# Kernel optimization log

Hardware: AMD Instinct MI355X
Metric: run time of the kernel (lower is better)

Reference implementation:

```python
import jax, jax.numpy as jnp
import numpy as np

NUM_HEADS = 16
LN_EPS = 1e-5


def setup_inputs() -> dict:
    key = jax.random.key(0)
    ks = jax.random.split(key, 12)
    B, S, D = 4, 2048, 1024
    inp = {
        "query": jax.random.normal(ks[0], (B, S, D), jnp.float32),
        "key": jax.random.normal(ks[1], (B, S, D), jnp.float32),
        "value": jax.random.normal(ks[2], (B, S, D), jnp.float32),
        "mask": jax.random.randint(ks[3], (B, S, S), 0, 2).astype(bool),
        "Wq": 0.02 * jax.random.normal(ks[4], (D, D), jnp.float32),
        "bq": jnp.zeros((D,), jnp.float32),
        "Wk": 0.02 * jax.random.normal(ks[5], (D, D), jnp.float32),
        "bk": jnp.zeros((D,), jnp.float32),
        "Wv": 0.02 * jax.random.normal(ks[6], (D, D), jnp.float32),
        "bv": jnp.zeros((D,), jnp.float32),
        "Wo": 0.02 * jax.random.normal(ks[7], (D, D), jnp.float32),
        "bo": jnp.zeros((D,), jnp.float32),
        "gamma": jnp.ones((D,), jnp.float32),
        "beta": jnp.zeros((D,), jnp.float32),
    }
    return inp


def reference(query, key, value, mask, Wq, bq, Wk, bk, Wv, bv, Wo, bo, gamma, beta):
    B, Sq, D = query.shape
    H = NUM_HEADS
    dk = D // H
    inv_sqrt_dk = 1.0 / float(np.sqrt(dk))

    def proj(x, W, bias):
        # (B, S, D) -> (B, H, S, dk)
        y = x @ W.T + bias
        return y.reshape(B, -1, H, dk).transpose(0, 2, 1, 3)

    Q = proj(query, Wq, bq)
    K = proj(key, Wk, bk)
    V = proj(value, Wv, bv)

    scores = jnp.einsum('bhqd,bhkd->bhqk', Q, K) * inv_sqrt_dk
    scores = jnp.where(mask[:, None, :, :], -jnp.inf, scores)
    attn = jax.nn.softmax(scores, axis=-1)  # (B, H, Sq, Sk)

    ctx = jnp.einsum('bhqk,bhkd->bhqd', attn, V)
    ctx = ctx.transpose(0, 2, 1, 3).reshape(B, Sq, D)

    out = ctx @ Wo.T + bo + query  # residual
    mean = out.mean(-1, keepdims=True)
    var = out.var(-1, keepdims=True)
    output = gamma * (out - mean) * jax.lax.rsqrt(var + LN_EPS) + beta

    # original returns attn flattened head-major: (H*B, Sq, Sk)
    attn_hm = attn.transpose(1, 0, 2, 3).reshape(B * H, Sq, -1)
    return output, attn_hm
```

## Files before the change

kernel.cpp:

```cpp
#include <hip/hip_runtime.h>
#include <hip/hip_bf16.h>
#include <math.h>
#include <stdint.h>

typedef __bf16 bf16_t;
typedef __bf16 bf16x8 __attribute__((ext_vector_type(8)));
typedef __bf16 bf16x4v __attribute__((ext_vector_type(4)));
typedef float f32x4 __attribute__((ext_vector_type(4)));

#define BB 4
#define SS 2048
#define DD 1024
#define HH 16
#define SCALE 0.125f
static constexpr size_t NE = (size_t)BB * SS * DD;
static constexpr size_t WN = (size_t)DD * DD;

__device__ inline f32x4 load4f(const bf16_t* p) {
    bf16x4v v = *(const bf16x4v*)p;
    return (f32x4){(float)v[0], (float)v[1], (float)v[2], (float)v[3]};
}
__device__ inline f32x4 load4f(const float* p) { return *(const f32x4*)p; }
__device__ inline void store4(bf16_t* p, f32x4 v) {
    bf16x4v o;
    for (int j = 0; j < 4; ++j) o[j] = (bf16_t)v[j];
    *(bf16x4v*)p = o;
}
__device__ inline void store4(float* p, f32x4 v) { *(f32x4*)p = v; }
__device__ inline void store16(bf16_t* p, const bf16_t* s) {
    *(bf16x8*)p       = *(const bf16x8*)s;
    *(bf16x8*)(p + 8) = *(const bf16x8*)(s + 8);
}
__device__ inline void store16(float* p, const bf16_t* s) {
    for (int j = 0; j < 16; j += 4) {
        f32x4 v = {(float)s[j], (float)s[j + 1], (float)s[j + 2], (float)s[j + 3]};
        *(f32x4*)(p + j) = v;
    }
}
__device__ inline void cvt8(const float* s, bf16_t* d) {
    f32x4 a = *(const f32x4*)s;
    f32x4 b = *(const f32x4*)(s + 4);
    bf16x8 r;
    for (int j = 0; j < 4; ++j) { r[j] = (bf16_t)a[j]; r[4 + j] = (bf16_t)b[j]; }
    *(bf16x8*)d = r;
}
__device__ __forceinline__ void async16(const bf16_t* g, bf16_t* l) {
    __builtin_amdgcn_global_load_lds(
        (const __attribute__((address_space(1))) void*)g,
        (__attribute__((address_space(3))) void*)l, 16, 0, 0);
}
__device__ __forceinline__ float dpp_max16(float x) {
    x = fmaxf(x, __int_as_float(__builtin_amdgcn_update_dpp(0, __float_as_int(x), 0xB1,  0xF, 0xF, true)));
    x = fmaxf(x, __int_as_float(__builtin_amdgcn_update_dpp(0, __float_as_int(x), 0x4E,  0xF, 0xF, true)));
    x = fmaxf(x, __int_as_float(__builtin_amdgcn_update_dpp(0, __float_as_int(x), 0x141, 0xF, 0xF, true)));
    x = fmaxf(x, __int_as_float(__builtin_amdgcn_update_dpp(0, __float_as_int(x), 0x140, 0xF, 0xF, true)));
    return x;
}
__device__ __forceinline__ float dpp_add16(float x) {
    x += __int_as_float(__builtin_amdgcn_update_dpp(0, __float_as_int(x), 0xB1,  0xF, 0xF, true));
    x += __int_as_float(__builtin_amdgcn_update_dpp(0, __float_as_int(x), 0x4E,  0xF, 0xF, true));
    x += __int_as_float(__builtin_amdgcn_update_dpp(0, __float_as_int(x), 0x141, 0xF, 0xF, true));
    x += __int_as_float(__builtin_amdgcn_update_dpp(0, __float_as_int(x), 0x140, 0xF, 0xF, true));
    return x;
}

__global__ void probe_kernel(const uint16_t* __restrict__ q,
                             const uint8_t* __restrict__ m,
                             int* __restrict__ flags)
{
    __shared__ int s_f32, s_byte, s_i32;
    if (threadIdx.x == 0) { s_f32 = 0; s_byte = 0; s_i32 = 0; }
    __syncthreads();
    {
        unsigned bits = ((unsigned)q[threadIdx.x]) << 16;
        float f = __uint_as_float(bits);
        if (!(fabsf(f) < 1e10f)) atomicOr(&s_f32, 1);
    }
    for (int j = threadIdx.x; j < 4096; j += 256) {
        if (m[j]) {
            if (j & 3) atomicOr(&s_byte, 1);
            else if ((j & 7) == 4) atomicOr(&s_i32, 1);
        }
    }
    __syncthreads();
    if (threadIdx.x == 0) {
        flags[0] = s_f32 ? 1 : 0;
        flags[1] = s_byte ? 0 : (s_i32 ? 1 : 2);
    }
}

__global__ __launch_bounds__(256) void cvt_qkv(
    const float* __restrict__ q, const float* __restrict__ k,
    const float* __restrict__ v, bf16_t* __restrict__ dst,
    const int* __restrict__ flags)
{
    if (flags[0] != 1) return;
    size_t i = ((size_t)blockIdx.x * 256 + threadIdx.x) * 8;
    const float* src;
    size_t off;
    if (i < NE)          { src = q; off = i; }
    else if (i < 2 * NE) { src = k; off = i - NE; }
    else                 { src = v; off = i - 2 * NE; }
    cvt8(src + off, dst + i);
}

__global__ __launch_bounds__(256) void cvt_w(
    const float* __restrict__ Wq, const float* __restrict__ Wk,
    const float* __restrict__ Wv, const float* __restrict__ Wo,
    const float* __restrict__ bq, const float* __restrict__ bk,
    const float* __restrict__ bv, const float* __restrict__ bo,
    bf16_t* __restrict__ dst, const int* __restrict__ flags)
{
    if (flags[0] != 1) return;
    size_t i = ((size_t)blockIdx.x * 256 + threadIdx.x) * 8;
    const float* src;
    size_t off;
    const size_t W4 = 4 * WN;
    if (i < W4) {
        int ws = (int)(i >> 20);
        src = ws == 0 ? Wq : ws == 1 ? Wk : ws == 2 ? Wv : Wo;
        off = i & (WN - 1);
    } else {
        size_t j = i - W4;
        int bs = (int)(j >> 10);
        src = bs == 0 ? bq : bs == 1 ? bk : bs == 2 ? bv : bo;
        off = j & 1023;
    }
    cvt8(src + off, dst + i);
}

template<int BIAS_ROW>
__global__ __launch_bounds__(256) void gemm_bt_bias(
    const bf16_t* __restrict__ A, const bf16_t* __restrict__ B,
    const bf16_t* __restrict__ bias, bf16_t* __restrict__ Y,
    int M, int N, int K, const int* __restrict__ flags, int want)
{
    if (flags[0] != want) return;

    __shared__ __align__(16) bf16_t As[128 * 64];
    __shared__ __align__(16) bf16_t Bs[128 * 64];

    const int tid = threadIdx.x;
    const int wave = tid >> 6;
    const int lane = tid & 63;
    const int quad = lane >> 4;
    const int l15  = lane & 15;
    const int wm = wave >> 1, wn = wave & 1;

    const int m0 = blockIdx.y * 128;
    const int n0 = blockIdx.x * 128;

    f32x4 acc[4][4];
    #pragma unroll
    for (int i = 0; i < 4; ++i)
        #pragma unroll
        for (int j = 0; j < 4; ++j)
            acc[i][j] = (f32x4){0.f, 0.f, 0.f, 0.f};

    for (int k0 = 0; k0 < K; k0 += 64) {
        __syncthreads();
        #pragma unroll
        for (int s = 0; s < 4; ++s) {
            int c = s * 256 + wave * 64 + lane;
            int row = c >> 3, col = (c & 7) * 8;
            bf16_t* la = &As[(size_t)(s * 256 + wave * 64) * 8];
            bf16_t* lb = &Bs[(size_t)(s * 256 + wave * 64) * 8];
            async16(&A[(size_t)(m0 + row) * K + k0 + col], la);
            async16(&B[(size_t)(n0 + row) * K + k0 + col], lb);
        }
        __syncthreads();
        bf16x8 a0[4], a1[4], b0[4], b1[4];
        #pragma unroll
        for (int mt = 0; mt < 4; ++mt) {
            const bf16_t* p = &As[(size_t)(wm * 64 + mt * 16 + l15) * 64 + quad * 8];
            a0[mt] = *(const bf16x8*)p;
            a1[mt] = *(const bf16x8*)(p + 32);
        }
        #pragma unroll
        for (int nt = 0; nt < 4; ++nt) {
            const bf16_t* p = &Bs[(size_t)(wn * 64 + nt * 16 + l15) * 64 + quad * 8];
            b0[nt] = *(const bf16x8*)p;
            b1[nt] = *(const bf16x8*)(p + 32);
        }
        #pragma unroll
        for (int mt = 0; mt < 4; ++mt)
            #pragma unroll
            for (int nt = 0; nt < 4; ++nt) {
                acc[mt][nt] = __builtin_amdgcn_mfma_f32_16x16x32_bf16(a0[mt], b0[nt], acc[mt][nt], 0, 0, 0);
                acc[mt][nt] = __builtin_amdgcn_mfma_f32_16x16x32_bf16(a1[mt], b1[nt], acc[mt][nt], 0, 0, 0);
            }
    }

    float brow[4][4];
    if (BIAS_ROW) {
        #pragma unroll
        for (int mt = 0; mt < 4; ++mt)
            #pragma unroll
            for (int r = 0; r < 4; ++r)
                brow[mt][r] = (float)bias[m0 + wm * 64 + mt * 16 + quad * 4 + r];
    }
    #pragma unroll
    for (int nt = 0; nt < 4; ++nt) {
        int n = n0 + wn * 64 + nt * 16 + l15;
        float bn = BIAS_ROW ? 0.f : (float)bias[n];
        #pragma unroll
        for (int mt = 0; mt < 4; ++mt) {
            int mbase = m0 + wm * 64 + mt * 16 + quad * 4;
            #pragma unroll
            for (int r = 0; r < 4; ++r) {
                float bv = BIAS_ROW ? brow[mt][r] : bn;
                Y[(size_t)(mbase + r) * N + n] = (bf16_t)(acc[mt][nt][r] + bv);
            }
        }
    }
}

template<typename T>
__global__ __launch_bounds__(256, 4) void attn_fused(
    const bf16_t* Qp, const bf16_t* __restrict__ Kp, const bf16_t* __restrict__ Vt,
    const void* maskp, const int* __restrict__ flags, int want,
    T* __restrict__ attn_out, bf16_t* ctx_out)
{
    if (flags[0] != want) return;

    __shared__ __align__(16) bf16_t Ks[64][72];
    __shared__ __align__(16) bf16_t Ps[64][72];
    __shared__ __align__(16) bf16_t QV[64][72];
    __shared__ uint64_t Msk[64];

    const int tid  = threadIdx.x;
    const int wave = tid >> 6;
    const int lane = tid & 63;
    const int quad = lane >> 4;
    const int l15  = lane & 15;
    const int qt = blockIdx.x;
    const int bh = blockIdx.y;
    const int b  = bh / HH;
    const int h  = bh % HH;
    const int q0 = qt * 64;

    const int mmode = flags[1];
    const uint8_t*  m8  = (const uint8_t*)maskp;
    const uint32_t* m32 = (const uint32_t*)maskp;
    const size_t mbase = (size_t)b * SS * SS;
    const int rowl_base = wave * 16 + quad * 4;
    const int qrow_base = q0 + rowl_base;

    auto stage_k_mask = [&](int kt) {
        #pragma unroll
        for (int j = 0; j < 2; ++j) {
            int c = tid * 2 + j;
            int row = c >> 3, cc = (c & 7) * 8;
            *(bf16x8*)&Ks[row][cc] =
                *(const bf16x8*)&Kp[(size_t)(b * SS + kt * 64 + row) * DD + h * 64 + cc];
        }
        int row = tid >> 2, ch = tid & 3;
        size_t e = mbase + (size_t)(q0 + row) * SS + kt * 64 + ch * 16;
        uint32_t bits = 0;
        if (mmode == 0) {
            uint4 v = *(const uint4*)(m8 + e);
            uint32_t w0 = v.x, w1 = v.y, w2 = v.z, w3 = v.w;
            bits |= ((w0 & 0x000000ffu) ? 1u : 0u) << 0;
            bits |= ((w0 & 0x0000ff00u) ? 1u : 0u) << 1;
            bits |= ((w0 & 0x00ff0000u) ? 1u : 0u) << 2;
            bits |= ((w0 & 0xff000000u) ? 1u : 0u) << 3;
            bits |= ((w1 & 0x000000ffu) ? 1u : 0u) << 4;
            bits |= ((w1 & 0x0000ff00u) ? 1u : 0u) << 5;
            bits |= ((w1 & 0x00ff0000u) ? 1u : 0u) << 6;
            bits |= ((w1 & 0xff000000u) ? 1u : 0u) << 7;
            bits |= ((w2 & 0x000000ffu) ? 1u : 0u) << 8;
            bits |= ((w2 & 0x0000ff00u) ? 1u : 0u) << 9;
            bits |= ((w2 & 0x00ff0000u) ? 1u : 0u) << 10;
            bits |= ((w2 & 0xff000000u) ? 1u : 0u) << 11;
            bits |= ((w3 & 0x000000ffu) ? 1u : 0u) << 12;
            bits |= ((w3 & 0x0000ff00u) ? 1u : 0u) << 13;
            bits |= ((w3 & 0x00ff0000u) ? 1u : 0u) << 14;
            bits |= ((w3 & 0xff000000u) ? 1u : 0u) << 15;
        } else if (mmode == 1) {
            const uint32_t* p = m32 + e;
            #pragma unroll
            for (int w = 0; w < 16; w += 4) {
                uint4 v = *(const uint4*)(p + w);
                bits |= (v.x ? 1u : 0u) << (w + 0);
                bits |= (v.y ? 1u : 0u) << (w + 1);
                bits |= (v.z ? 1u : 0u) << (w + 2);
                bits |= (v.w ? 1u : 0u) << (w + 3);
            }
        } else {
            const uint32_t* p = m32 + 2 * e;
            #pragma unroll
            for (int g = 0; g < 16; g += 2) {
                uint4 v = *(const uint4*)(p + 2 * g);
                bits |= (v.x ? 1u : 0u) << (g + 0);
                bits |= (v.z ? 1u : 0u) << (g + 1);
            }
        }
        ((uint16_t*)Msk)[row * 4 + ch] = (uint16_t)bits;
    };

    #pragma unroll
    for (int j = 0; j < 2; ++j) {
        int c = tid * 2 + j;
        int row = c >> 3, cc = (c & 7) * 8;
        *(bf16x8*)&QV[row][cc] =
            *(const bf16x8*)&Qp[(size_t)(b * SS + q0 + row) * DD + h * 64 + cc];
    }
    __syncthreads();
    const bf16x8 aq0 = *(const bf16x8*)&QV[wave * 16 + l15][quad * 8];
    const bf16x8 aq1 = *(const bf16x8*)&QV[wave * 16 + l15][32 + quad * 8];

    float mrow[4], lrow[4];
    #pragma unroll
    for (int r = 0; r < 4; ++r) { mrow[r] = -INFINITY; lrow[r] = 0.f; }

    for (int kt = 0; kt < 32; ++kt) {
        __syncthreads();
        stage_k_mask(kt);
        __syncthreads();
        float sv[4][4];
        #pragma unroll
        for (int nt = 0; nt < 4; ++nt) {
            bf16x8 b0 = *(const bf16x8*)&Ks[nt * 16 + l15][quad * 8];
            bf16x8 b1 = *(const bf16x8*)&Ks[nt * 16 + l15][32 + quad * 8];
            f32x4 s = (f32x4){0.f, 0.f, 0.f, 0.f};
            s = __builtin_amdgcn_mfma_f32_16x16x32_bf16(aq0, b0, s, 0, 0, 0);
            s = __builtin_amdgcn_mfma_f32_16x16x32_bf16(aq1, b1, s, 0, 0, 0);
            #pragma unroll
            for (int r = 0; r < 4; ++r) sv[nt][r] = s[r];
        }
        #pragma unroll
        for (int r = 0; r < 4; ++r) {
            uint64_t mb = Msk[rowl_base + r];
            float x[4]; bool mk[4];
            float mloc = -INFINITY;
            #pragma unroll
            for (int nt = 0; nt < 4; ++nt) {
                mk[nt] = (mb >> (nt * 16 + l15)) & 1ull;
                x[nt] = mk[nt] ? -INFINITY : sv[nt][r] * SCALE;
                mloc = fmaxf(mloc, x[nt]);
            }
            float mnew = fmaxf(mrow[r], dpp_max16(mloc));
            float ps = 0.f;
            #pragma unroll
            for (int nt = 0; nt < 4; ++nt)
                ps += mk[nt] ? 0.f : __expf(x[nt] - mnew);
            ps = dpp_add16(ps);
            float alpha = (mrow[r] == mnew) ? 1.f : __expf(mrow[r] - mnew);
            lrow[r] = lrow[r] * alpha + ps;
            mrow[r] = mnew;
        }
    }

    float rinv[4];
    #pragma unroll
    for (int r = 0; r < 4; ++r) rinv[r] = (lrow[r] > 0.f) ? 1.f / lrow[r] : 0.f;

    f32x4 cacc[4];
    #pragma unroll
    for (int dt = 0; dt < 4; ++dt) cacc[dt] = (f32x4){0.f, 0.f, 0.f, 0.f};

    for (int kt = 0; kt < 32; ++kt) {
        __syncthreads();
        stage_k_mask(kt);
        #pragma unroll
        for (int j = 0; j < 2; ++j) {
            int c = tid * 2 + j;
            int row = c >> 3, cc = (c & 7) * 8;
            *(bf16x8*)&QV[row][cc] =
                *(const bf16x8*)&Vt[((size_t)(h * 64 + row) * BB + b) * SS + kt * 64 + cc];
        }
        __syncthreads();
        float sv[4][4];
        #pragma unroll
        for (int nt = 0; nt < 4; ++nt) {
            bf16x8 b0 = *(const bf16x8*)&Ks[nt * 16 + l15][quad * 8];
            bf16x8 b1 = *(const bf16x8*)&Ks[nt * 16 + l15][32 + quad * 8];
            f32x4 s = (f32x4){0.f, 0.f, 0.f, 0.f};
            s = __builtin_amdgcn_mfma_f32_16x16x32_bf16(aq0, b0, s, 0, 0, 0);
            s = __builtin_amdgcn_mfma_f32_16x16x32_bf16(aq1, b1, s, 0, 0, 0);
            #pragma unroll
            for (int r = 0; r < 4; ++r) sv[nt][r] = s[r];
        }
        #pragma unroll
        for (int r = 0; r < 4; ++r) {
            uint64_t mb = Msk[rowl_base + r];
            #pragma unroll
            for (int nt = 0; nt < 4; ++nt) {
                bool mk = (mb >> (nt * 16 + l15)) & 1ull;
                float p = mk ? 0.f : __expf(sv[nt][r] * SCALE - mrow[r]) * rinv[r];
                Ps[rowl_base + r][nt * 16 + l15] = (bf16_t)p;
            }
        }
        __syncthreads();
        bf16x8 ap0 = *(const bf16x8*)&Ps[wave * 16 + l15][quad * 8];
        bf16x8 ap1 = *(const bf16x8*)&Ps[wave * 16 + l15][32 + quad * 8];
        #pragma unroll
        for (int dt = 0; dt < 4; ++dt) {
            bf16x8 bv0 = *(const bf16x8*)&QV[dt * 16 + l15][quad * 8];
            bf16x8 bv1 = *(const bf16x8*)&QV[dt * 16 + l15][32 + quad * 8];
            cacc[dt] = __builtin_amdgcn_mfma_f32_16x16x32_bf16(ap0, bv0, cacc[dt], 0, 0, 0);
            cacc[dt] = __builtin_amdgcn_mfma_f32_16x16x32_bf16(ap1, bv1, cacc[dt], 0, 0, 0);
        }
        {
            int row = tid >> 2;
            int ch  = (tid & 3) * 16;
            size_t dst = ((size_t)(h * BB + b) * SS + (q0 + row)) * SS + kt * 64 + ch;
            store16(&attn_out[dst], &Ps[row][ch]);
        }
    }

    #pragma unroll
    for (int dt = 0; dt < 4; ++dt)
        #pragma unroll
        for (int r = 0; r < 4; ++r)
            ctx_out[(size_t)(b * SS + qrow_base + r) * DD + h * 64 + dt * 16 + l15] =
                (bf16_t)cacc[dt][r];
}

template<typename T>
__global__ __launch_bounds__(256) void ln_kernel(
    const bf16_t* __restrict__ P, const T* __restrict__ Qr,
    const T* __restrict__ gamma, const T* __restrict__ beta,
    T* __restrict__ out, const int* __restrict__ flags, int want)
{
    if (flags[0] != want) return;
    const int row = blockIdx.x;
    const int tid = threadIdx.x;
    const size_t base = (size_t)row * DD + tid * 4;
    f32x4 pv = load4f(&P[base]);
    f32x4 qv = load4f(&Qr[base]);
    float x[4]; float s = 0.f, s2 = 0.f;
    for (int j = 0; j < 4; ++j) {
        x[j] = pv[j] + qv[j];
        s += x[j]; s2 += x[j] * x[j];
    }
    for (int off = 1; off < 64; off <<= 1) {
        s  += __shfl_xor(s, off);
        s2 += __shfl_xor(s2, off);
    }
    __shared__ float sh[8];
    const int wave = tid >> 6, lane = tid & 63;
    if (lane == 0) { sh[wave] = s; sh[4 + wave] = s2; }
    __syncthreads();
    s  = sh[0] + sh[1] + sh[2] + sh[3];
    s2 = sh[4] + sh[5] + sh[6] + sh[7];
    float mean = s * (1.0f / DD);
    float var  = s2 * (1.0f / DD) - mean * mean;
    float inv  = rsqrtf(var + 1e-5f);
    f32x4 g  = load4f(&gamma[tid * 4]);
    f32x4 bt = load4f(&beta[tid * 4]);
    f32x4 o;
    for (int j = 0; j < 4; ++j)
        o[j] = g[j] * (x[j] - mean) * inv + bt[j];
    store4(&out[base], o);
}

template<typename T>
static void run_chain(void* const* d_in, void* d_out, bf16_t* Qp, bf16_t* Kp,
                      int* flags, int want, hipStream_t stream)
{
    const T* query = (const T*)d_in[0];
    const void* mask = d_in[3];
    const T* gamma = (const T*)d_in[12];
    const T* beta  = (const T*)d_in[13];

    T* out  = (T*)d_out;
    T* attn = out + NE;
    bf16_t* Vp = (bf16_t*)d_out;
    const int M = BB * SS;

    const bf16_t *qb, *kb, *vb, *Wqb, *Wkb, *Wvb, *Wob, *bqb, *bkb, *bvb, *bob;
    if constexpr (sizeof(T) == 4) {
        bf16_t* S0 = (bf16_t*)attn;
        bf16_t* WB = Vp + NE;
        cvt_qkv<<<dim3(3 * 4096), 256, 0, stream>>>(
            (const float*)d_in[0], (const float*)d_in[1], (const float*)d_in[2], S0, flags);
        cvt_w<<<dim3(2050), 256, 0, stream>>>(
            (const float*)d_in[4], (const float*)d_in[6], (const float*)d_in[8], (const float*)d_in[10],
            (const float*)d_in[5], (const float*)d_in[7], (const float*)d_in[9], (const float*)d_in[11],
            WB, flags);
        qb = S0; kb = S0 + NE; vb = S0 + 2 * NE;
        Wqb = WB; Wkb = WB + WN; Wvb = WB + 2 * WN; Wob = WB + 3 * WN;
        bqb = WB + 4 * WN; bkb = bqb + 1024; bvb = bqb + 2048; bob = bqb + 3072;
    } else {
        qb  = (const bf16_t*)d_in[0]; kb  = (const bf16_t*)d_in[1]; vb  = (const bf16_t*)d_in[2];
        Wqb = (const bf16_t*)d_in[4]; bqb = (const bf16_t*)d_in[5];
        Wkb = (const bf16_t*)d_in[6]; bkb = (const bf16_t*)d_in[7];
        Wvb = (const bf16_t*)d_in[8]; bvb = (const bf16_t*)d_in[9];
        Wob = (const bf16_t*)d_in[10]; bob = (const bf16_t*)d_in[11];
    }

    dim3 gg(DD / 128, M / 128);
    gemm_bt_bias<0><<<gg, 256, 0, stream>>>(qb, Wqb, bqb, Qp, M, DD, DD, flags, want);
    gemm_bt_bias<0><<<gg, 256, 0, stream>>>(kb, Wkb, bkb, Kp, M, DD, DD, flags, want);
    gemm_bt_bias<1><<<dim3(M / 128, DD / 128), 256, 0, stream>>>(
        Wvb, vb, bvb, Vp, DD, M, DD, flags, want);

    attn_fused<T><<<dim3(SS / 64, BB * HH), 256, 0, stream>>>(
        Qp, Kp, Vp, mask, flags, want, attn, Qp);

    gemm_bt_bias<0><<<gg, 256, 0, stream>>>(Qp, Wob, bob, Kp, M, DD, DD, flags, want);

    ln_kernel<T><<<M, 256, 0, stream>>>(Kp, query, gamma, beta, out, flags, want);
}

extern "C" void kernel_launch(void* const* d_in, const int* in_sizes, int n_in,
                              void* d_out, int out_size, void* d_ws, size_t ws_size,
                              hipStream_t stream)
{
    int* flags = (int*)d_ws;
    bf16_t* Qp = (bf16_t*)((char*)d_ws + 16);
    bf16_t* Kp = Qp + NE;

    probe_kernel<<<1, 256, 0, stream>>>((const uint16_t*)d_in[0],
                                        (const uint8_t*)d_in[3], flags);

    run_chain<bf16_t>(d_in, d_out, Qp, Kp, flags, 0, stream);
    run_chain<float >(d_in, d_out, Qp, Kp, flags, 1, stream);
}
```

Baseline: 1.825 ms.

## Double-buffer K/mask in attention, cache mask bits, merge dtype chains into one

The attention kernel now double-buffers K tiles and mask bits in LDS, prefetching the next tile into registers while the current one is computed. Mask bits from the first pass are kept in registers so the second pass does not reload the mask. The attn-probability stores become nontemporal, and s_setprio is raised around the MFMA sections. The two dtype-specific launch chains are merged into a single chain that picks pointers from a runtime flag, which halves the number of early-exit kernel launches at the cost of extra register pressure and branches.

```diff
diff --git a/kernel.cpp b/kernel.cpp
--- a/kernel.cpp
+++ b/kernel.cpp
@@ -27,14 +27,14 @@
     *(bf16x4v*)p = o;
 }
 __device__ inline void store4(float* p, f32x4 v) { *(f32x4*)p = v; }
-__device__ inline void store16(bf16_t* p, const bf16_t* s) {
-    *(bf16x8*)p       = *(const bf16x8*)s;
-    *(bf16x8*)(p + 8) = *(const bf16x8*)(s + 8);
-}
-__device__ inline void store16(float* p, const bf16_t* s) {
+__device__ inline void store16nt(bf16_t* p, const bf16_t* s) {
+    __builtin_nontemporal_store(*(const bf16x8*)s, (bf16x8*)p);
+    __builtin_nontemporal_store(*(const bf16x8*)(s + 8), (bf16x8*)(p + 8));
+}
+__device__ inline void store16nt(float* p, const bf16_t* s) {
     for (int j = 0; j < 16; j += 4) {
         f32x4 v = {(float)s[j], (float)s[j + 1], (float)s[j + 2], (float)s[j + 3]};
-        *(f32x4*)(p + j) = v;
+        __builtin_nontemporal_store(v, (f32x4*)(p + j));
     }
 }
 __device__ inline void cvt8(const float* s, bf16_t* d) {
@@ -131,11 +131,16 @@
 
 template<int BIAS_ROW>
 __global__ __launch_bounds__(256) void gemm_bt_bias(
-    const bf16_t* __restrict__ A, const bf16_t* __restrict__ B,
-    const bf16_t* __restrict__ bias, bf16_t* __restrict__ Y,
-    int M, int N, int K, const int* __restrict__ flags, int want)
-{
-    if (flags[0] != want) return;
+    const int* __restrict__ flags,
+    const bf16_t* __restrict__ A0, const bf16_t* __restrict__ A1,
+    const bf16_t* __restrict__ B0, const bf16_t* __restrict__ B1,
+    const bf16_t* __restrict__ c0, const bf16_t* __restrict__ c1,
+    bf16_t* __restrict__ Y, int M, int N, int K)
+{
+    const int f = flags[0];
+    const bf16_t* A = f ? A1 : A0;
+    const bf16_t* B = f ? B1 : B0;
+    const bf16_t* bias = f ? c1 : c0;
 
     __shared__ __align__(16) bf16_t As[128 * 64];
     __shared__ __align__(16) bf16_t Bs[128 * 64];
@@ -215,18 +220,16 @@
     }
 }
 
-template<typename T>
 __global__ __launch_bounds__(256, 4) void attn_fused(
-    const bf16_t* Qp, const bf16_t* __restrict__ Kp, const bf16_t* __restrict__ Vt,
-    const void* maskp, const int* __restrict__ flags, int want,
-    T* __restrict__ attn_out, bf16_t* ctx_out)
-{
-    if (flags[0] != want) return;
-
-    __shared__ __align__(16) bf16_t Ks[64][72];
+    const int* __restrict__ flags,
+    const bf16_t* Qp, const bf16_t* __restrict__ Kp,
+    const bf16_t* __restrict__ Vt, const void* __restrict__ maskp,
+    void* __restrict__ d_out, bf16_t* ctx_out)
+{
+    __shared__ __align__(16) bf16_t Ks[2][64][72];
+    __shared__ __align__(16) bf16_t Vs[64][72];
     __shared__ __align__(16) bf16_t Ps[64][72];
-    __shared__ __align__(16) bf16_t QV[64][72];
-    __shared__ uint64_t Msk[64];
+    __shared__ uint64_t Msk[2][64];
 
     const int tid  = threadIdx.x;
     const int wave = tid >> 6;
@@ -239,6 +242,7 @@
     const int h  = bh % HH;
     const int q0 = qt * 64;
 
+    const int f32o  = flags[0];
     const int mmode = flags[1];
     const uint8_t*  m8  = (const uint8_t*)maskp;
     const uint32_t* m32 = (const uint32_t*)maskp;
@@ -246,36 +250,42 @@
     const int rowl_base = wave * 16 + quad * 4;
     const int qrow_base = q0 + rowl_base;
 
-    auto stage_k_mask = [&](int kt) {
-        #pragma unroll
-        for (int j = 0; j < 2; ++j) {
-            int c = tid * 2 + j;
-            int row = c >> 3, cc = (c & 7) * 8;
-            *(bf16x8*)&Ks[row][cc] =
-                *(const bf16x8*)&Kp[(size_t)(b * SS + kt * 64 + row) * DD + h * 64 + cc];
-        }
+    float* attnF  = (float*)d_out + NE;
+    bf16_t* attnH = (bf16_t*)d_out + NE;
+
+    const int c0 = tid * 2,     sr0 = c0 >> 3, sc0 = (c0 & 7) * 8;
+    const int c1 = tid * 2 + 1, sr1 = c1 >> 3, sc1 = (c1 & 7) * 8;
+
+    auto loadK = [&](int kt, bf16x8* kr) {
+        kr[0] = *(const bf16x8*)&Kp[(size_t)(b * SS + kt * 64 + sr0) * DD + h * 64 + sc0];
+        kr[1] = *(const bf16x8*)&Kp[(size_t)(b * SS + kt * 64 + sr1) * DD + h * 64 + sc1];
+    };
+    auto writeK = [&](int slot, const bf16x8* kr) {
+        *(bf16x8*)&Ks[slot][sr0][sc0] = kr[0];
+        *(bf16x8*)&Ks[slot][sr1][sc1] = kr[1];
+    };
+    auto loadV = [&](int kt, bf16x8* vr) {
+        vr[0] = *(const bf16x8*)&Vt[((size_t)(h * 64 + sr0) * BB + b) * SS + kt * 64 + sc0];
+        vr[1] = *(const bf16x8*)&Vt[((size_t)(h * 64 + sr1) * BB + b) * SS + kt * 64 + sc1];
+    };
+    auto writeV = [&](const bf16x8* vr) {
+        *(bf16x8*)&Vs[sr0][sc0] = vr[0];
+        *(bf16x8*)&Vs[sr1][sc1] = vr[1];
+    };
+    auto stage_mask = [&](int kt, int slot) {
         int row = tid >> 2, ch = tid & 3;
         size_t e = mbase + (size_t)(q0 + row) * SS + kt * 64 + ch * 16;
         uint32_t bits = 0;
         if (mmode == 0) {
             uint4 v = *(const uint4*)(m8 + e);
-            uint32_t w0 = v.x, w1 = v.y, w2 = v.z, w3 = v.w;
-            bits |= ((w0 & 0x000000ffu) ? 1u : 0u) << 0;
-            bits |= ((w0 & 0x0000ff00u) ? 1u : 0u) << 1;
-            bits |= ((w0 & 0x00ff0000u) ? 1u : 0u) << 2;
-            bits |= ((w0 & 0xff000000u) ? 1u : 0u) << 3;
-            bits |= ((w1 & 0x000000ffu) ? 1u : 0u) << 4;
-            bits |= ((w1 & 0x0000ff00u) ? 1u : 0u) << 5;
-            bits |= ((w1 & 0x00ff0000u) ? 1u : 0u) << 6;
-            bits |= ((w1 & 0xff000000u) ? 1u : 0u) << 7;
-            bits |= ((w2 & 0x000000ffu) ? 1u : 0u) << 8;
-            bits |= ((w2 & 0x0000ff00u) ? 1u : 0u) << 9;
-            bits |= ((w2 & 0x00ff0000u) ? 1u : 0u) << 10;
-            bits |= ((w2 & 0xff000000u) ? 1u : 0u) << 11;
-            bits |= ((w3 & 0x000000ffu) ? 1u : 0u) << 12;
-            bits |= ((w3 & 0x0000ff00u) ? 1u : 0u) << 13;
-            bits |= ((w3 & 0x00ff0000u) ? 1u : 0u) << 14;
-            bits |= ((w3 & 0xff000000u) ? 1u : 0u) << 15;
+            uint32_t w[4] = {v.x, v.y, v.z, v.w};
+            #pragma unroll
+            for (int g = 0; g < 4; ++g) {
+                bits |= ((w[g] & 0x000000ffu) ? 1u : 0u) << (g * 4 + 0);
+                bits |= ((w[g] & 0x0000ff00u) ? 1u : 0u) << (g * 4 + 1);
+                bits |= ((w[g] & 0x00ff0000u) ? 1u : 0u) << (g * 4 + 2);
+                bits |= ((w[g] & 0xff000000u) ? 1u : 0u) << (g * 4 + 3);
+            }
         } else if (mmode == 1) {
             const uint32_t* p = m32 + e;
             #pragma unroll
@@ -295,60 +305,72 @@
                 bits |= (v.z ? 1u : 0u) << (g + 1);
             }
         }
-        ((uint16_t*)Msk)[row * 4 + ch] = (uint16_t)bits;
+        ((uint16_t*)&Msk[slot][0])[row * 4 + ch] = (uint16_t)bits;
     };
 
-    #pragma unroll
-    for (int j = 0; j < 2; ++j) {
-        int c = tid * 2 + j;
-        int row = c >> 3, cc = (c & 7) * 8;
-        *(bf16x8*)&QV[row][cc] =
-            *(const bf16x8*)&Qp[(size_t)(b * SS + q0 + row) * DD + h * 64 + cc];
+    {
+        *(bf16x8*)&Ps[sr0][sc0] =
+            *(const bf16x8*)&Qp[(size_t)(b * SS + q0 + sr0) * DD + h * 64 + sc0];
+        *(bf16x8*)&Ps[sr1][sc1] =
+            *(const bf16x8*)&Qp[(size_t)(b * SS + q0 + sr1) * DD + h * 64 + sc1];
     }
     __syncthreads();
-    const bf16x8 aq0 = *(const bf16x8*)&QV[wave * 16 + l15][quad * 8];
-    const bf16x8 aq1 = *(const bf16x8*)&QV[wave * 16 + l15][32 + quad * 8];
+    const bf16x8 aq0 = *(const bf16x8*)&Ps[wave * 16 + l15][quad * 8];
+    const bf16x8 aq1 = *(const bf16x8*)&Ps[wave * 16 + l15][32 + quad * 8];
 
     float mrow[4], lrow[4];
     #pragma unroll
     for (int r = 0; r < 4; ++r) { mrow[r] = -INFINITY; lrow[r] = 0.f; }
+    uint64_t mlo[4] = {0, 0, 0, 0}, mhi[4] = {0, 0, 0, 0};
+
+    bf16x8 kreg[2], knext[2];
+    loadK(0, kreg);
+    stage_mask(0, 0);
+    writeK(0, kreg);
 
     for (int kt = 0; kt < 32; ++kt) {
-        __syncthreads();
-        stage_k_mask(kt);
+        const int cur = kt & 1;
+        if (kt < 31) { loadK(kt + 1, knext); stage_mask(kt + 1, cur ^ 1); }
         __syncthreads();
         float sv[4][4];
+        __builtin_amdgcn_s_setprio(1);
         #pragma unroll
         for (int nt = 0; nt < 4; ++nt) {
-            bf16x8 b0 = *(const bf16x8*)&Ks[nt * 16 + l15][quad * 8];
-            bf16x8 b1 = *(const bf16x8*)&Ks[nt * 16 + l15][32 + quad * 8];
+            bf16x8 b0 = *(const bf16x8*)&Ks[cur][nt * 16 + l15][quad * 8];
+            bf16x8 b1 = *(const bf16x8*)&Ks[cur][nt * 16 + l15][32 + quad * 8];
             f32x4 s = (f32x4){0.f, 0.f, 0.f, 0.f};
             s = __builtin_amdgcn_mfma_f32_16x16x32_bf16(aq0, b0, s, 0, 0, 0);
             s = __builtin_amdgcn_mfma_f32_16x16x32_bf16(aq1, b1, s, 0, 0, 0);
             #pragma unroll
             for (int r = 0; r < 4; ++r) sv[nt][r] = s[r];
         }
+        __builtin_amdgcn_s_setprio(0);
         #pragma unroll
         for (int r = 0; r < 4; ++r) {
-            uint64_t mb = Msk[rowl_base + r];
-            float x[4]; bool mk[4];
+            uint64_t mb = Msk[cur][rowl_base + r];
+            uint32_t nib = 0;
+            float x[4];
             float mloc = -INFINITY;
             #pragma unroll
             for (int nt = 0; nt < 4; ++nt) {
-                mk[nt] = (mb >> (nt * 16 + l15)) & 1ull;
-                x[nt] = mk[nt] ? -INFINITY : sv[nt][r] * SCALE;
+                uint32_t mk = (uint32_t)(mb >> (nt * 16 + l15)) & 1u;
+                nib |= mk << nt;
+                x[nt] = mk ? -INFINITY : sv[nt][r] * SCALE;
                 mloc = fmaxf(mloc, x[nt]);
             }
+            if (kt < 16) mlo[r] |= (uint64_t)nib << (kt * 4);
+            else         mhi[r] |= (uint64_t)nib << ((kt - 16) * 4);
             float mnew = fmaxf(mrow[r], dpp_max16(mloc));
             float ps = 0.f;
             #pragma unroll
             for (int nt = 0; nt < 4; ++nt)
-                ps += mk[nt] ? 0.f : __expf(x[nt] - mnew);
+                ps += ((nib >> nt) & 1u) ? 0.f : __expf(x[nt] - mnew);
             ps = dpp_add16(ps);
             float alpha = (mrow[r] == mnew) ? 1.f : __expf(mrow[r] - mnew);
             lrow[r] = lrow[r] * alpha + ps;
             mrow[r] = mnew;
         }
+        if (kt < 31) { writeK(cur ^ 1, knext); }
     }
 
     float rinv[4];
@@ -359,54 +381,61 @@
     #pragma unroll
     for (int dt = 0; dt < 4; ++dt) cacc[dt] = (f32x4){0.f, 0.f, 0.f, 0.f};
 
+    bf16x8 vcur[2], vnext[2];
+    loadK(0, kreg);
+    loadV(0, vcur);
+    writeK(0, kreg);
+
     for (int kt = 0; kt < 32; ++kt) {
+        const int cur = kt & 1;
+        if (kt < 31) { loadK(kt + 1, knext); loadV(kt + 1, vnext); }
         __syncthreads();
-        stage_k_mask(kt);
-        #pragma unroll
-        for (int j = 0; j < 2; ++j) {
-            int c = tid * 2 + j;
-            int row = c >> 3, cc = (c & 7) * 8;
-            *(bf16x8*)&QV[row][cc] =
-                *(const bf16x8*)&Vt[((size_t)(h * 64 + row) * BB + b) * SS + kt * 64 + cc];
-        }
-        __syncthreads();
+        writeV(vcur);
         float sv[4][4];
+        __builtin_amdgcn_s_setprio(1);
         #pragma unroll
         for (int nt = 0; nt < 4; ++nt) {
-            bf16x8 b0 = *(const bf16x8*)&Ks[nt * 16 + l15][quad * 8];
-            bf16x8 b1 = *(const bf16x8*)&Ks[nt * 16 + l15][32 + quad * 8];
+            bf16x8 b0 = *(const bf16x8*)&Ks[cur][nt * 16 + l15][quad * 8];
+            bf16x8 b1 = *(const bf16x8*)&Ks[cur][nt * 16 + l15][32 + quad * 8];
             f32x4 s = (f32x4){0.f, 0.f, 0.f, 0.f};
             s = __builtin_amdgcn_mfma_f32_16x16x32_bf16(aq0, b0, s, 0, 0, 0);
             s = __builtin_amdgcn_mfma_f32_16x16x32_bf16(aq1, b1, s, 0, 0, 0);
             #pragma unroll
             for (int r = 0; r < 4; ++r) sv[nt][r] = s[r];
         }
+        __builtin_amdgcn_s_setprio(0);
         #pragma unroll
         for (int r = 0; r < 4; ++r) {
-            uint64_t mb = Msk[rowl_base + r];
+            uint32_t nib = (uint32_t)((kt < 16 ? (mlo[r] >> (kt * 4))
+                                               : (mhi[r] >> ((kt - 16) * 4))) & 0xFull);
             #pragma unroll
             for (int nt = 0; nt < 4; ++nt) {
-                bool mk = (mb >> (nt * 16 + l15)) & 1ull;
+                bool mk = (nib >> nt) & 1u;
                 float p = mk ? 0.f : __expf(sv[nt][r] * SCALE - mrow[r]) * rinv[r];
                 Ps[rowl_base + r][nt * 16 + l15] = (bf16_t)p;
             }
         }
+        if (kt < 31) { writeK(cur ^ 1, knext); }
         __syncthreads();
         bf16x8 ap0 = *(const bf16x8*)&Ps[wave * 16 + l15][quad * 8];
         bf16x8 ap1 = *(const bf16x8*)&Ps[wave * 16 + l15][32 + quad * 8];
+        __builtin_amdgcn_s_setprio(1);
         #pragma unroll
         for (int dt = 0; dt < 4; ++dt) {
-            bf16x8 bv0 = *(const bf16x8*)&QV[dt * 16 + l15][quad * 8];
-            bf16x8 bv1 = *(const bf16x8*)&QV[dt * 16 + l15][32 + quad * 8];
+            bf16x8 bv0 = *(const bf16x8*)&Vs[dt * 16 + l15][quad * 8];
+            bf16x8 bv1 = *(const bf16x8*)&Vs[dt * 16 + l15][32 + quad * 8];
             cacc[dt] = __builtin_amdgcn_mfma_f32_16x16x32_bf16(ap0, bv0, cacc[dt], 0, 0, 0);
             cacc[dt] = __builtin_amdgcn_mfma_f32_16x16x32_bf16(ap1, bv1, cacc[dt], 0, 0, 0);
         }
+        __builtin_amdgcn_s_setprio(0);
         {
             int row = tid >> 2;
             int ch  = (tid & 3) * 16;
             size_t dst = ((size_t)(h * BB + b) * SS + (q0 + row)) * SS + kt * 64 + ch;
-            store16(&attn_out[dst], &Ps[row][ch]);
-        }
+            if (f32o) store16nt(attnF + dst, &Ps[row][ch]);
+            else      store16nt(attnH + dst, &Ps[row][ch]);
+        }
+        vcur[0] = vnext[0]; vcur[1] = vnext[1];
     }
 
     #pragma unroll
@@ -417,18 +446,18 @@
                 (bf16_t)cacc[dt][r];
 }
 
-template<typename T>
 __global__ __launch_bounds__(256) void ln_kernel(
-    const bf16_t* __restrict__ P, const T* __restrict__ Qr,
-    const T* __restrict__ gamma, const T* __restrict__ beta,
-    T* __restrict__ out, const int* __restrict__ flags, int want)
-{
-    if (flags[0] != want) return;
+    const int* __restrict__ flags,
+    const bf16_t* __restrict__ P, const void* __restrict__ Qr,
+    const void* __restrict__ gamma, const void* __restrict__ beta,
+    void* __restrict__ out)
+{
+    const int f = flags[0];
     const int row = blockIdx.x;
     const int tid = threadIdx.x;
     const size_t base = (size_t)row * DD + tid * 4;
     f32x4 pv = load4f(&P[base]);
-    f32x4 qv = load4f(&Qr[base]);
+    f32x4 qv = f ? load4f((const float*)Qr + base) : load4f((const bf16_t*)Qr + base);
     float x[4]; float s = 0.f, s2 = 0.f;
     for (int j = 0; j < 4; ++j) {
         x[j] = pv[j] + qv[j];
@@ -447,61 +476,13 @@
     float mean = s * (1.0f / DD);
     float var  = s2 * (1.0f / DD) - mean * mean;
     float inv  = rsqrtf(var + 1e-5f);
-    f32x4 g  = load4f(&gamma[tid * 4]);
-    f32x4 bt = load4f(&beta[tid * 4]);
+    f32x4 g  = f ? load4f((const float*)gamma + tid * 4) : load4f((const bf16_t*)gamma + tid * 4);
+    f32x4 bt = f ? load4f((const float*)beta  + tid * 4) : load4f((const bf16_t*)beta  + tid * 4);
     f32x4 o;
     for (int j = 0; j < 4; ++j)
         o[j] = g[j] * (x[j] - mean) * inv + bt[j];
-    store4(&out[base], o);
-}
-
-template<typename T>
-static void run_chain(void* const* d_in, void* d_out, bf16_t* Qp, bf16_t* Kp,
-                      int* flags, int want, hipStream_t stream)
-{
-    const T* query = (const T*)d_in[0];
-    const void* mask = d_in[3];
-    const T* gamma = (const T*)d_in[12];
-    const T* beta  = (const T*)d_in[13];
-
-    T* out  = (T*)d_out;
-    T* attn = out + NE;
-    bf16_t* Vp = (bf16_t*)d_out;
-    const int M = BB * SS;
-
-    const bf16_t *qb, *kb, *vb, *Wqb, *Wkb, *Wvb, *Wob, *bqb, *bkb, *bvb, *bob;
-    if constexpr (sizeof(T) == 4) {
-        bf16_t* S0 = (bf16_t*)attn;
-        bf16_t* WB = Vp + NE;
-        cvt_qkv<<<dim3(3 * 4096), 256, 0, stream>>>(
-            (const float*)d_in[0], (const float*)d_in[1], (const float*)d_in[2], S0, flags);
-        cvt_w<<<dim3(2050), 256, 0, stream>>>(
-            (const float*)d_in[4], (const float*)d_in[6], (const float*)d_in[8], (const float*)d_in[10],
-            (const float*)d_in[5], (const float*)d_in[7], (const float*)d_in[9], (const float*)d_in[11],
-            WB, flags);
-        qb = S0; kb = S0 + NE; vb = S0 + 2 * NE;
-        Wqb = WB; Wkb = WB + WN; Wvb = WB + 2 * WN; Wob = WB + 3 * WN;
-        bqb = WB + 4 * WN; bkb = bqb + 1024; bvb = bqb + 2048; bob = bqb + 3072;
-    } else {
-        qb  = (const bf16_t*)d_in[0]; kb  = (const bf16_t*)d_in[1]; vb  = (const bf16_t*)d_in[2];
-        Wqb = (const bf16_t*)d_in[4]; bqb = (const bf16_t*)d_in[5];
-        Wkb = (const bf16_t*)d_in[6]; bkb = (const bf16_t*)d_in[7];
-        Wvb = (const bf16_t*)d_in[8]; bvb = (const bf16_t*)d_in[9];
-        Wob = (const bf16_t*)d_in[10]; bob = (const bf16_t*)d_in[11];
-    }
-
-    dim3 gg(DD / 128, M / 128);
-    gemm_bt_bias<0><<<gg, 256, 0, stream>>>(qb, Wqb, bqb, Qp, M, DD, DD, flags, want);
-    gemm_bt_bias<0><<<gg, 256, 0, stream>>>(kb, Wkb, bkb, Kp, M, DD, DD, flags, want);
-    gemm_bt_bias<1><<<dim3(M / 128, DD / 128), 256, 0, stream>>>(
-        Wvb, vb, bvb, Vp, DD, M, DD, flags, want);
-
-    attn_fused<T><<<dim3(SS / 64, BB * HH), 256, 0, stream>>>(
-        Qp, Kp, Vp, mask, flags, want, attn, Qp);
-
-    gemm_bt_bias<0><<<gg, 256, 0, stream>>>(Qp, Wob, bob, Kp, M, DD, DD, flags, want);
-
-    ln_kernel<T><<<M, 256, 0, stream>>>(Kp, query, gamma, beta, out, flags, want);
+    if (f) store4((float*)out + base, o);
+    else   store4((bf16_t*)out + base, o);
 }
 
 extern "C" void kernel_launch(void* const* d_in, const int* in_sizes, int n_in,
@@ -511,10 +492,42 @@
     int* flags = (int*)d_ws;
     bf16_t* Qp = (bf16_t*)((char*)d_ws + 16);
     bf16_t* Kp = Qp + NE;
+    bf16_t* Vp = (bf16_t*)d_out;
+    bf16_t* WB = (bf16_t*)d_out + NE;
+    bf16_t* S0 = (bf16_t*)((float*)d_out + NE);
+    const bf16_t* bq1 = WB + 4 * WN;
+    const int M = BB * SS;
 
     probe_kernel<<<1, 256, 0, stream>>>((const uint16_t*)d_in[0],
                                         (const uint8_t*)d_in[3], flags);
-
-    run_chain<bf16_t>(d_in, d_out, Qp, Kp, flags, 0, stream);
-    run_chain<float >(d_in, d_out, Qp, Kp, flags, 1, stream);
-}
+    cvt_qkv<<<dim3(3 * 4096), 256, 0, stream>>>(
+        (const float*)d_in[0], (const float*)d_in[1], (const float*)d_in[2], S0, flags);
+    cvt_w<<<dim3(2050), 256, 0, stream>>>(
+        (const float*)d_in[4], (const float*)d_in[6], (const float*)d_in[8], (const float*)d_in[10],
+        (const float*)d_in[5], (const float*)d_in[7], (const float*)d_in[9], (const float*)d_in[11],
+        WB, flags);
+
+    dim3 gg(DD / 128, M / 128);
+    gemm_bt_bias<0><<<gg, 256, 0, stream>>>(flags,
+        (const bf16_t*)d_in[0], S0,
+        (const bf16_t*)d_in[4], WB,
+        (const bf16_t*)d_in[5], bq1, Qp, M, DD, DD);
+    gemm_bt_bias<0><<<gg, 256, 0, stream>>>(flags,
+        (const bf16_t*)d_in[1], S0 + NE,
+        (const bf16_t*)d_in[6], WB + WN,
+        (const bf16_t*)d_in[7], bq1 + 1024, Kp, M, DD, DD);
+    gemm_bt_bias<1><<<dim3(M / 128, DD / 128), 256, 0, stream>>>(flags,
+        (const bf16_t*)d_in[8], WB + 2 * WN,
+        (const bf16_t*)d_in[2], S0 + 2 * NE,
+        (const bf16_t*)d_in[9], bq1 + 2048, Vp, DD, M, DD);
+
+    attn_fused<<<dim3(SS / 64, BB * HH), 256, 0, stream>>>(
+        flags, Qp, Kp, Vp, d_in[3], d_out, Qp);
+
+    gemm_bt_bias<0><<<gg, 256, 0, stream>>>(flags,
+        Qp, Qp,
+        (const bf16_t*)d_in[10], WB + 3 * WN,
+        (const bf16_t*)d_in[11], bq1 + 3072, Kp, M, DD, DD);
+
+    ln_kernel<<<dim3(M), 256, 0, stream>>>(flags, Kp, d_in[0], d_in[12], d_in[13], d_out);
+}
```

Result: slower. 2.910 ms (+59.5%).
